# Kernel optimization log

Hardware: AMD Instinct MI355X
Metric: run time of the kernel (lower is better)

Reference implementation:

```python
import jax, jax.numpy as jnp
import numpy as np

T, B, OBS, H, M1, M2, A = 64, 2048, 48, 256, 512, 256, 12
LOG2PI = float(np.log(2.0 * np.pi))
LOG_STD_MIN, LOG_STD_MAX = -5.0, 2.0
LN_EPS = 1e-5


def _elu(x):
    return jnp.where(x > 0, x, jnp.expm1(x))


def setup_inputs() -> dict:
    key = jax.random.key(0)
    ks = jax.random.split(key, 10)
    s = lambda k, shape, sc=0.05: jax.random.normal(k, shape, jnp.float32) * sc
    return dict(
        x=jax.random.normal(ks[0], (T, B, OBS), jnp.float32),
        done=jax.random.randint(ks[1], (T, B), 0, 2).astype(jnp.int32),
        h0=jnp.zeros((B, H), jnp.float32),
        c0=jnp.zeros((B, H), jnp.float32),
        W_ih=s(ks[2], (4 * H, OBS)),
        W_hh=s(ks[3], (4 * H, H)),
        b_ih=jnp.zeros((4 * H,), jnp.float32),
        b_hh=jnp.zeros((4 * H,), jnp.float32),
        ln_g=jnp.ones((H,), jnp.float32),
        ln_b=jnp.zeros((H,), jnp.float32),
        W1=s(ks[4], (H, M1)),
        b1=jnp.zeros((M1,), jnp.float32),
        W2=s(ks[5], (M1, M2)),
        b2=jnp.zeros((M2,), jnp.float32),
        Wm=s(ks[6], (M2, A), 0.01),
        bm=jnp.zeros((A,), jnp.float32),
        Ws=s(ks[7], (M2, A), 0.01),
        bs=jnp.zeros((A,), jnp.float32),
    )


def reference(x, h0, c0, W_ih, W_hh, b_ih, b_hh, ln_g, ln_b,
              W1, b1, W2, b2, Wm, bm, Ws, bs, done):
    # Precompute input-side gate projections for all timesteps: [T, B, 4H]
    xg = jnp.einsum('tbi,gi->tbg', x, W_ih) + b_ih + b_hh
    keep = 1.0 - done.astype(jnp.float32)  # [T, B]; reset state where done==1

    def step(carry, inp):
        h, c = carry
        xgt, m = inp
        h = h * m[:, None]
        c = c * m[:, None]
        g = xgt + h @ W_hh.T  # [B, 4H], PyTorch gate order i,f,g,o
        i, f, gg, o = jnp.split(g, 4, axis=-1)
        c = jax.nn.sigmoid(f) * c + jax.nn.sigmoid(i) * jnp.tanh(gg)
        h = jax.nn.sigmoid(o) * jnp.tanh(c)
        return (h, c), h

    (_, _), hs = jax.lax.scan(step, (h0, c0), (xg, keep))
    hflat = hs.reshape(T * B, H)

    # LayerNorm
    mu = hflat.mean(-1, keepdims=True)
    var = ((hflat - mu) ** 2).mean(-1, keepdims=True)
    y = (hflat - mu) / jnp.sqrt(var + LN_EPS) * ln_g + ln_b

    # Actor MLP (ELU after every Linear, per build_mlp)
    y = _elu(y @ W1 + b1)
    y = _elu(y @ W2 + b2)

    mean = y @ Wm + bm
    logstd = jnp.clip(y @ Ws + bs, LOG_STD_MIN, LOG_STD_MAX)
    # deterministic action == mean, so (a - mu)^2 / (2 sigma^2) == 0
    logp = (-logstd - 0.5 * LOG2PI).sum(-1)
    ent = (0.5 + 0.5 * LOG2PI + logstd).sum(-1)
    # [T*B, A+2]: action mean, log_prob, entropy
    return jnp.concatenate([mean, logp[:, None], ent[:, None]], axis=-1)
```

## Files before the change

kernel.cpp:

```cpp
#include <hip/hip_runtime.h>
#include <hip/hip_bf16.h>
#include <math.h>

#define T_   64
#define B_   2048
#define OBS_ 48
#define H_   256
#define M1_  512
#define M2_  256
#define A_   12
#define BH_  (B_ * H_)
#define KP_  320
#define GROUPS_  128
#define SLICES_  2
#define RPB_     16

typedef unsigned short u16;
typedef unsigned long long u64;
typedef __attribute__((ext_vector_type(8))) short bf16x8;
typedef __attribute__((ext_vector_type(4))) float f32x4;

static __device__ __forceinline__ u16 f2b(float f) {
    __hip_bfloat16 h = __float2bfloat16(f);
    return *reinterpret_cast<u16*>(&h);
}
static __device__ __forceinline__ float b2f(u16 u) {
    union { unsigned u32v; float f; } v; v.u32v = ((unsigned)u) << 16; return v.f;
}
static __device__ __forceinline__ float sigm(float x) {
    return 1.0f / (1.0f + __expf(-x));
}
static __device__ __forceinline__ float tanh_fast(float x) {
    x = fminf(fmaxf(x, -15.0f), 15.0f);
    float e = __expf(2.0f * x);
    return (e - 1.0f) / (e + 1.0f);
}
static __device__ __forceinline__ float elu(float x) {
    return x > 0.0f ? x : (__expf(x) - 1.0f);
}

__global__ void prep_xpad(const float* __restrict__ x, u16* __restrict__ xpad,
                          unsigned* __restrict__ cnt) {
    if (blockIdx.x == 0 && threadIdx.x < GROUPS_ * SLICES_) cnt[threadIdx.x] = 0;
    const int gid = blockIdx.x * 256 + threadIdx.x;
    const int r = gid >> 3, k0 = (gid & 7) * 8;
    u16 tmp[8];
    if (k0 < OBS_) {
        const float4 f0 = *(const float4*)(x + (size_t)r * OBS_ + k0);
        const float4 f1 = *(const float4*)(x + (size_t)r * OBS_ + k0 + 4);
        tmp[0] = f2b(f0.x); tmp[1] = f2b(f0.y); tmp[2] = f2b(f0.z); tmp[3] = f2b(f0.w);
        tmp[4] = f2b(f1.x); tmp[5] = f2b(f1.y); tmp[6] = f2b(f1.z); tmp[7] = f2b(f1.w);
    } else {
        #pragma unroll
        for (int i = 0; i < 8; ++i) tmp[i] = 0;
    }
    *(uint4*)(xpad + (size_t)gid * 8) = *(uint4*)tmp;
}

__global__ void prep_weights(const float* __restrict__ W_ih, const float* __restrict__ W_hh,
                             const float* __restrict__ W1,  const float* __restrict__ W2,
                             const float* __restrict__ Wm,  const float* __restrict__ Ws,
                             u16* __restrict__ Wcat, u16* __restrict__ W1T,
                             u16* __restrict__ W2T,  u16* __restrict__ WhT) {
    const int b = blockIdx.x, tid = threadIdx.x;
    if (b < 1024) {
        const int s = b >> 9, w = (b >> 6) & 7, g = (b >> 4) & 3, jj = b & 15;
        const int src = g * 256 + s * 128 + w * 16 + jj;
        for (int k = tid; k < KP_; k += 256) {
            float v;
            if (k < OBS_)     v = W_ih[src * OBS_ + k];
            else if (k < 64)  v = 0.0f;
            else if (k < 192) v = W_hh[src * H_ + s * 128 + (k - 64)];
            else              v = W_hh[src * H_ + (1 - s) * 128 + (k - 192)];
            Wcat[b * KP_ + k] = f2b(v);
        }
    } else if (b < 1536) {
        const int n = b - 1024;
        W1T[n * 256 + tid] = f2b(W1[tid * M1_ + n]);
    } else if (b < 1792) {
        const int n = b - 1536;
        W2T[n * 512 + tid]       = f2b(W2[tid * M2_ + n]);
        W2T[n * 512 + tid + 256] = f2b(W2[(tid + 256) * M2_ + n]);
    } else {
        const int n = b - 1792;
        float v = 0.0f;
        if (n < 12)                 v = Wm[tid * A_ + n];
        else if (n >= 16 && n < 28) v = Ws[tid * A_ + (n - 16)];
        WhT[n * 256 + tid] = f2b(v);
    }
}

#define ASM_(row, chunk) (a_sm + (size_t)(row) * 320 + (size_t)(((chunk) ^ ((row) & 7)) << 3))

__global__ __launch_bounds__(512, 2) void lstm_sync2(
    const u16*  __restrict__ xpad,
    const int*  __restrict__ done,
    const float* __restrict__ h0,
    const float* __restrict__ c0,
    u16*        __restrict__ hs,
    const u16*  __restrict__ Wcat,
    const float* __restrict__ b_ih,
    const float* __restrict__ b_hh,
    unsigned*   __restrict__ cnt)
{
    __shared__ u16 a_sm[RPB_ * 320];
    __shared__ unsigned okf;

    const int tid  = threadIdx.x;
    const int lane = tid & 63;
    const int w    = tid >> 6;
    const int quad = lane >> 4, l16 = lane & 15;
    const int grp  = blockIdx.x >> 1;
    const int s    = blockIdx.x & 1;
    const int b0   = grp * RPB_;
    const int j    = s * 128 + w * 16 + l16;
    const int jrel = w * 16 + l16;
    const int pc0  = (1 - s) * 128;

    float bsum[4];
    #pragma unroll
    for (int g = 0; g < 4; ++g) bsum[g] = b_ih[g * 256 + j] + b_hh[g * 256 + j];

    float cst[4];
    #pragma unroll
    for (int r = 0; r < 4; ++r) {
        const int row = b0 + quad * 4 + r;
        cst[r] = done[row] ? 0.0f : c0[(size_t)row * H_ + j];
    }

    bf16x8 Bs[4][10];
    #pragma unroll
    for (int g = 0; g < 4; ++g) {
        const u16* wp = Wcat + (size_t)(((s * 8 + w) * 4 + g) * 16 + l16) * KP_ + quad * 8;
        #pragma unroll
        for (int kt = 0; kt < 10; ++kt)
            Bs[g][kt] = *(const bf16x8*)(wp + kt * 32);
    }

    if ((tid & 3) == 0) {
        const int idx = tid >> 2, row = idx >> 3, seg = idx & 7;
        *(uint4*)ASM_(row, seg) =
            *(const uint4*)(xpad + (size_t)(b0 + row) * 64 + seg * 8);
    }
    {
        const int row = tid >> 5, c8 = tid & 31;
        const int cglob = c8 * 8;
        const int dn = done[b0 + row];
        const float* hr = h0 + (size_t)(b0 + row) * H_ + cglob;
        u16 tmp[8];
        #pragma unroll
        for (int e = 0; e < 8; ++e) tmp[e] = dn ? (u16)0 : f2b(hr[e]);
        const int chunk = (((cglob >> 7) == s) ? 8 : 24) + ((cglob & 127) >> 3);
        *(uint4*)ASM_(row, chunk) = *(uint4*)tmp;
    }
    __syncthreads();

    for (int t = 0; t < T_; ++t) {
        unsigned fv = 0;
        if (tid == 0 && t > 0)
            fv = __hip_atomic_load(&cnt[blockIdx.x ^ 1], __ATOMIC_RELAXED,
                                   __HIP_MEMORY_SCOPE_AGENT);

        f32x4 acc[4];
        #pragma unroll
        for (int g = 0; g < 4; ++g) acc[g] = (f32x4){0, 0, 0, 0};
        #pragma unroll
        for (int kt = 0; kt < 6; ++kt) {
            const bf16x8 af = *(const bf16x8*)ASM_(l16, kt * 4 + quad);
            #pragma unroll
            for (int g = 0; g < 4; ++g)
                acc[g] = __builtin_amdgcn_mfma_f32_16x16x32_bf16(af, Bs[g][kt], acc[g], 0, 0, 0);
        }

        if (tid == 0) okf = (t == 0 || fv >= (unsigned)t) ? 1u : 0u;
        __syncthreads();
        {
            int guard = 0;
            while (!okf) {
                if (tid == 0) {
                    __builtin_amdgcn_s_sleep(1);
                    fv = __hip_atomic_load(&cnt[blockIdx.x ^ 1], __ATOMIC_RELAXED,
                                           __HIP_MEMORY_SCOPE_AGENT);
                    if (fv >= (unsigned)t || ++guard > (1 << 22)) okf = 1u;
                }
                __syncthreads();
            }
        }

        if (t > 0 && tid < 256) {
            const u16* hst = hs + (size_t)t * BH_;
            const int row = tid >> 4, q = tid & 15;
            const int dn = done[(size_t)t * B_ + b0 + row];
            uint4 hv = *(const uint4*)(hst + (size_t)(b0 + row) * H_ + pc0 + q * 8);
            if (dn) hv = make_uint4(0u, 0u, 0u, 0u);
            *(uint4*)ASM_(row, 24 + q) = hv;
        }
        if (t + 1 < T_ && tid >= 256 && tid < 384) {
            const int idx = tid - 256, row = idx >> 3, seg = idx & 7;
            *(uint4*)ASM_(row, seg) =
                *(const uint4*)(xpad + ((size_t)(t + 1) * B_ + b0 + row) * 64 + seg * 8);
        }
        __syncthreads();

        #pragma unroll
        for (int kt = 6; kt < 10; ++kt) {
            const bf16x8 af = *(const bf16x8*)ASM_(l16, kt * 4 + quad);
            #pragma unroll
            for (int g = 0; g < 4; ++g)
                acc[g] = __builtin_amdgcn_mfma_f32_16x16x32_bf16(af, Bs[g][kt], acc[g], 0, 0, 0);
        }

        u16* hs1 = hs + (size_t)(t + 1) * BH_;
        #pragma unroll
        for (int r = 0; r < 4; ++r) {
            const int rowl = quad * 4 + r;
            const int rowg = b0 + rowl;
            const float gi = acc[0][r] + bsum[0];
            const float gf = acc[1][r] + bsum[1];
            const float gg = acc[2][r] + bsum[2];
            const float go = acc[3][r] + bsum[3];
            const float cn = sigm(gf) * cst[r] + sigm(gi) * tanh_fast(gg);
            const float h  = sigm(go) * tanh_fast(cn);
            const float kp = (t + 1 < T_)
                ? (done[(size_t)(t + 1) * B_ + rowg] ? 0.0f : 1.0f) : 1.0f;
            cst[r] = cn * kp;
            const int e = 64 + jrel;
            *(ASM_(rowl, e >> 3) + (e & 7)) = f2b(h * kp);
            const unsigned hb = (unsigned)f2b(h);
            const unsigned ob = (unsigned)__shfl_xor((int)hb, 1);
            if ((l16 & 1) == 0) {
                const unsigned val = hb | (ob << 16);
                __hip_atomic_store((unsigned*)(hs1 + (size_t)rowg * H_ + (j & ~1)), val,
                                   __ATOMIC_RELAXED, __HIP_MEMORY_SCOPE_AGENT);
            }
        }
        __syncthreads();

        if (tid == 0 && t + 1 < T_)
            __hip_atomic_store(&cnt[blockIdx.x], (unsigned)(t + 1),
                               __ATOMIC_RELAXED, __HIP_MEMORY_SCOPE_AGENT);
    }
}

#define SY(row, col) ((size_t)(row) * 256 + ((((col) >> 3) ^ ((row) & 7)) << 3) + ((col) & 7))

__global__ __launch_bounds__(512, 4) void mlp_mfma64(
    const u16*  __restrict__ hs,
    float*      __restrict__ out,
    const float* __restrict__ lng, const float* __restrict__ lnb,
    const u16*  __restrict__ W1T, const float* __restrict__ b1,
    const u16*  __restrict__ W2T, const float* __restrict__ b2,
    const u16*  __restrict__ WhT,
    const float* __restrict__ bm, const float* __restrict__ bs)
{
    __shared__ u16 ybf[64 * 256];
    __shared__ u16 yh [64 * 256];

    const int tid  = threadIdx.x;
    const int lane = tid & 63;
    const int wave = tid >> 6;
    const int quad = lane >> 4, l16 = lane & 15;
    const int row0 = blockIdx.x * 64;

    {
        const float4 gv = *(const float4*)(lng + lane * 4);
        const float4 bv = *(const float4*)(lnb + lane * 4);
        #pragma unroll
        for (int rr = 0; rr < 8; ++rr) {
            const int r = wave * 8 + rr;
            const u64 hv8 = __builtin_nontemporal_load(
                (const u64*)(hs + (size_t)(row0 + r) * H_ + lane * 4));
            const u16 h0v = (u16)(hv8 & 0xffff), h1v = (u16)((hv8 >> 16) & 0xffff);
            const u16 h2v = (u16)((hv8 >> 32) & 0xffff), h3v = (u16)(hv8 >> 48);
            const float v0 = b2f(h0v), v1 = b2f(h1v), v2 = b2f(h2v), v3 = b2f(h3v);
            float s  = v0 + v1 + v2 + v3;
            float ss = v0 * v0 + v1 * v1 + v2 * v2 + v3 * v3;
            #pragma unroll
            for (int off = 32; off > 0; off >>= 1) {
                s  += __shfl_down(s,  off);
                ss += __shfl_down(ss, off);
            }
            s = __shfl(s, 0); ss = __shfl(ss, 0);
            const float mu   = s * (1.0f / 256.0f);
            const float rstd = rsqrtf(ss * (1.0f / 256.0f) - mu * mu + 1e-5f);
            ushort4 o;
            o.x = f2b((v0 - mu) * rstd * gv.x + bv.x);
            o.y = f2b((v1 - mu) * rstd * gv.y + bv.y);
            o.z = f2b((v2 - mu) * rstd * gv.z + bv.z);
            o.w = f2b((v3 - mu) * rstd * gv.w + bv.w);
            *(ushort4*)(ybf + SY(r, lane * 4)) = o;
        }
    }
    __syncthreads();

    f32x4 acc2[4][2];
    #pragma unroll
    for (int m = 0; m < 4; ++m)
        #pragma unroll
        for (int j = 0; j < 2; ++j) acc2[m][j] = (f32x4){0,0,0,0};

    #pragma unroll
    for (int ph = 0; ph < 2; ++ph) {
        {
            f32x4 acc[4][2];
            #pragma unroll
            for (int m = 0; m < 4; ++m)
                #pragma unroll
                for (int j = 0; j < 2; ++j) acc[m][j] = (f32x4){0,0,0,0};
            const int n0 = ph * 256 + wave * 32;
            const u16* wp0 = W1T + (size_t)(n0 + l16) * 256 + quad * 8;
            const u16* wp1 = W1T + (size_t)(n0 + 16 + l16) * 256 + quad * 8;
            #pragma unroll
            for (int kt = 0; kt < 8; ++kt) {
                const int k0 = kt * 32;
                const bf16x8 bw0 = *(const bf16x8*)(wp0 + k0);
                const bf16x8 bw1 = *(const bf16x8*)(wp1 + k0);
                #pragma unroll
                for (int m = 0; m < 4; ++m) {
                    const bf16x8 af = *(const bf16x8*)(ybf + SY(m * 16 + l16, k0 + quad * 8));
                    acc[m][0] = __builtin_amdgcn_mfma_f32_16x16x32_bf16(af, bw0, acc[m][0], 0, 0, 0);
                    acc[m][1] = __builtin_amdgcn_mfma_f32_16x16x32_bf16(af, bw1, acc[m][1], 0, 0, 0);
                }
            }
            const float bb0 = b1[n0 + l16], bb1 = b1[n0 + 16 + l16];
            __syncthreads();
            #pragma unroll
            for (int m = 0; m < 4; ++m)
                #pragma unroll
                for (int r = 0; r < 4; ++r) {
                    const int row = m * 16 + quad * 4 + r;
                    yh[SY(row, wave * 32 + l16)]      = f2b(elu(acc[m][0][r] + bb0));
                    yh[SY(row, wave * 32 + 16 + l16)] = f2b(elu(acc[m][1][r] + bb1));
                }
        }
        __syncthreads();

        {
            const int n0 = wave * 32;
            const u16* wp0 = W2T + (size_t)(n0 + l16) * 512 + ph * 256 + quad * 8;
            const u16* wp1 = W2T + (size_t)(n0 + 16 + l16) * 512 + ph * 256 + quad * 8;
            #pragma unroll
            for (int kt = 0; kt < 8; ++kt) {
                const int k0 = kt * 32;
                const bf16x8 bw0 = *(const bf16x8*)(wp0 + k0);
                const bf16x8 bw1 = *(const bf16x8*)(wp1 + k0);
                #pragma unroll
                for (int m = 0; m < 4; ++m) {
                    const bf16x8 af = *(const bf16x8*)(yh + SY(m * 16 + l16, k0 + quad * 8));
                    acc2[m][0] = __builtin_amdgcn_mfma_f32_16x16x32_bf16(af, bw0, acc2[m][0], 0, 0, 0);
                    acc2[m][1] = __builtin_amdgcn_mfma_f32_16x16x32_bf16(af, bw1, acc2[m][1], 0, 0, 0);
                }
            }
        }
        __syncthreads();
    }

    {
        const float bb0 = b2[wave * 32 + l16], bb1 = b2[wave * 32 + 16 + l16];
        #pragma unroll
        for (int m = 0; m < 4; ++m)
            #pragma unroll
            for (int r = 0; r < 4; ++r) {
                const int row = m * 16 + quad * 4 + r;
                ybf[SY(row, wave * 32 + l16)]      = f2b(elu(acc2[m][0][r] + bb0));
                ybf[SY(row, wave * 32 + 16 + l16)] = f2b(elu(acc2[m][1][r] + bb1));
            }
    }
    __syncthreads();

    float* lsf = (float*)yh;
    if (wave < 4) {
        f32x4 a0 = {0,0,0,0}, a1 = {0,0,0,0};
        const u16* wp0 = WhT + (size_t)l16 * 256 + quad * 8;
        const u16* wp1 = WhT + (size_t)(16 + l16) * 256 + quad * 8;
        #pragma unroll
        for (int kt = 0; kt < 8; ++kt) {
            const int k0 = kt * 32;
            const bf16x8 af  = *(const bf16x8*)(ybf + SY(wave * 16 + l16, k0 + quad * 8));
            const bf16x8 bw0 = *(const bf16x8*)(wp0 + k0);
            const bf16x8 bw1 = *(const bf16x8*)(wp1 + k0);
            a0 = __builtin_amdgcn_mfma_f32_16x16x32_bf16(af, bw0, a0, 0, 0, 0);
            a1 = __builtin_amdgcn_mfma_f32_16x16x32_bf16(af, bw1, a1, 0, 0, 0);
        }
        if (l16 < 12) {
            const float bbm = bm[l16], bbs = bs[l16];
            #pragma unroll
            for (int r = 0; r < 4; ++r) {
                const int row = wave * 16 + quad * 4 + r;
                out[(size_t)(row0 + row) * 14 + l16] = a0[r] + bbm;
                lsf[row * 16 + l16] = fminf(fmaxf(a1[r] + bbs, -5.0f), 2.0f);
            }
        }
    }
    __syncthreads();
    if (tid < 64) {
        float s = 0.0f;
        #pragma unroll
        for (int q = 0; q < 12; ++q) s += lsf[tid * 16 + q];
        const float LOG2PI = 1.8378770664093453f;
        out[(size_t)(row0 + tid) * 14 + 12] = -s - 6.0f * LOG2PI;
        out[(size_t)(row0 + tid) * 14 + 13] =  s + 6.0f + 6.0f * LOG2PI;
    }
}

extern "C" void kernel_launch(void* const* d_in, const int* in_sizes, int n_in,
                              void* d_out, int out_size, void* d_ws, size_t ws_size,
                              hipStream_t stream) {
    (void)in_sizes; (void)n_in; (void)out_size; (void)ws_size;
    const float* x    = (const float*)d_in[0];
    const int*   done = (const int*)  d_in[1];
    const float* h0   = (const float*)d_in[2];
    const float* c0   = (const float*)d_in[3];
    const float* W_ih = (const float*)d_in[4];
    const float* W_hh = (const float*)d_in[5];
    const float* b_ih = (const float*)d_in[6];
    const float* b_hh = (const float*)d_in[7];
    const float* lng  = (const float*)d_in[8];
    const float* lnb  = (const float*)d_in[9];
    const float* W1   = (const float*)d_in[10];
    const float* b1   = (const float*)d_in[11];
    const float* W2   = (const float*)d_in[12];
    const float* b2   = (const float*)d_in[13];
    const float* Wm   = (const float*)d_in[14];
    const float* bm   = (const float*)d_in[15];
    const float* Ws   = (const float*)d_in[16];
    const float* bs   = (const float*)d_in[17];
    float* out = (float*)d_out;

    unsigned char* p = (unsigned char*)d_ws;
    u16* hs    = (u16*)p;              p += (size_t)(T_ + 1) * BH_ * 2;
    u16* xpad  = (u16*)p;              p += (size_t)T_ * B_ * 64 * 2;
    u16* Wcat  = (u16*)p;              p += (size_t)1024 * KP_ * 2;
    u16* W1T   = (u16*)p;              p += (size_t)M1_ * H_ * 2;
    u16* W2T   = (u16*)p;              p += (size_t)M2_ * M1_ * 2;
    u16* WhT   = (u16*)p;              p += (size_t)32 * H_ * 2;
    unsigned* cnt = (unsigned*)p;      p += 1024;

    prep_xpad<<<(T_ * B_ * 8) / 256, 256, 0, stream>>>(x, xpad, cnt);
    prep_weights<<<1824, 256, 0, stream>>>(W_ih, W_hh, W1, W2, Wm, Ws,
                                           Wcat, W1T, W2T, WhT);

    lstm_sync2<<<GROUPS_ * SLICES_, 512, 0, stream>>>(
        xpad, done, h0, c0, hs, Wcat, b_ih, b_hh, cnt);

    mlp_mfma64<<<(T_ * B_) / 64, 512, 0, stream>>>(
        hs + BH_, out, lng, lnb, W1T, b1, W2T, b2, WhT, bm, bs);
}
```

Before: 581.4 us.

## Restructure LSTM step sync: wait at step end, double-buffer x, prefetch h

The LSTM kernel now waits on the partner block's counter at the end of each step instead of mid-step. This removes the mid-step spin loop and one of the two block barriers per step. The x input is double-buffered in shared memory, and the partner's h slice and the next x tile are loaded into registers before the first MFMA batch, hiding global latency behind compute. The blocks are also remapped so partner slices are 128 blocks apart, and the two prep kernels are fused into one launch. The trade-offs are more shared memory per block and a reliance on the end-of-step wait to make the partner's hs writes visible to the early loads.

Result: slower. 598.1 us (+2.9%).

```diff
diff --git a/kernel.cpp b/kernel.cpp
--- a/kernel.cpp
+++ b/kernel.cpp
@@ -39,30 +39,32 @@
     return x > 0.0f ? x : (__expf(x) - 1.0f);
 }
 
-__global__ void prep_xpad(const float* __restrict__ x, u16* __restrict__ xpad,
-                          unsigned* __restrict__ cnt) {
-    if (blockIdx.x == 0 && threadIdx.x < GROUPS_ * SLICES_) cnt[threadIdx.x] = 0;
-    const int gid = blockIdx.x * 256 + threadIdx.x;
-    const int r = gid >> 3, k0 = (gid & 7) * 8;
-    u16 tmp[8];
-    if (k0 < OBS_) {
-        const float4 f0 = *(const float4*)(x + (size_t)r * OBS_ + k0);
-        const float4 f1 = *(const float4*)(x + (size_t)r * OBS_ + k0 + 4);
-        tmp[0] = f2b(f0.x); tmp[1] = f2b(f0.y); tmp[2] = f2b(f0.z); tmp[3] = f2b(f0.w);
-        tmp[4] = f2b(f1.x); tmp[5] = f2b(f1.y); tmp[6] = f2b(f1.z); tmp[7] = f2b(f1.w);
-    } else {
-        #pragma unroll
-        for (int i = 0; i < 8; ++i) tmp[i] = 0;
-    }
-    *(uint4*)(xpad + (size_t)gid * 8) = *(uint4*)tmp;
-}
-
-__global__ void prep_weights(const float* __restrict__ W_ih, const float* __restrict__ W_hh,
-                             const float* __restrict__ W1,  const float* __restrict__ W2,
-                             const float* __restrict__ Wm,  const float* __restrict__ Ws,
-                             u16* __restrict__ Wcat, u16* __restrict__ W1T,
-                             u16* __restrict__ W2T,  u16* __restrict__ WhT) {
-    const int b = blockIdx.x, tid = threadIdx.x;
+__global__ void prep_all(const float* __restrict__ x, u16* __restrict__ xpad,
+                         const float* __restrict__ W_ih, const float* __restrict__ W_hh,
+                         const float* __restrict__ W1,  const float* __restrict__ W2,
+                         const float* __restrict__ Wm,  const float* __restrict__ Ws,
+                         u16* __restrict__ Wcat, u16* __restrict__ W1T,
+                         u16* __restrict__ W2T,  u16* __restrict__ WhT,
+                         unsigned* __restrict__ cnt) {
+    const int blk = blockIdx.x, tid = threadIdx.x;
+    if (blk < 4096) {
+        const int gid = blk * 256 + tid;
+        const int r = gid >> 3, k0 = (gid & 7) * 8;
+        u16 tmp[8];
+        if (k0 < OBS_) {
+            const float4 f0 = *(const float4*)(x + (size_t)r * OBS_ + k0);
+            const float4 f1 = *(const float4*)(x + (size_t)r * OBS_ + k0 + 4);
+            tmp[0] = f2b(f0.x); tmp[1] = f2b(f0.y); tmp[2] = f2b(f0.z); tmp[3] = f2b(f0.w);
+            tmp[4] = f2b(f1.x); tmp[5] = f2b(f1.y); tmp[6] = f2b(f1.z); tmp[7] = f2b(f1.w);
+        } else {
+            #pragma unroll
+            for (int i = 0; i < 8; ++i) tmp[i] = 0;
+        }
+        *(uint4*)(xpad + (size_t)gid * 8) = *(uint4*)tmp;
+        return;
+    }
+    const int b = blk - 4096;
+    if (b == 0 && tid < GROUPS_ * SLICES_) cnt[tid] = 0;
     if (b < 1024) {
         const int s = b >> 9, w = (b >> 6) & 7, g = (b >> 4) & 3, jj = b & 15;
         const int src = g * 256 + s * 128 + w * 16 + jj;
@@ -90,9 +92,9 @@
     }
 }
 
-#define ASM_(row, chunk) (a_sm + (size_t)(row) * 320 + (size_t)(((chunk) ^ ((row) & 7)) << 3))
-
-__global__ __launch_bounds__(512, 2) void lstm_sync2(
+#define ASM_(row, chunk) (a_sm + (size_t)(row) * 384 + (size_t)(((chunk) ^ ((row) & 7)) << 3))
+
+__global__ __launch_bounds__(512, 2) void lstm_sync3(
     const u16*  __restrict__ xpad,
     const int*  __restrict__ done,
     const float* __restrict__ h0,
@@ -103,15 +105,15 @@
     const float* __restrict__ b_hh,
     unsigned*   __restrict__ cnt)
 {
-    __shared__ u16 a_sm[RPB_ * 320];
-    __shared__ unsigned okf;
+    __shared__ u16 a_sm[RPB_ * 384];
 
     const int tid  = threadIdx.x;
     const int lane = tid & 63;
     const int w    = tid >> 6;
     const int quad = lane >> 4, l16 = lane & 15;
-    const int grp  = blockIdx.x >> 1;
-    const int s    = blockIdx.x & 1;
+    const int grp  = blockIdx.x & 127;
+    const int s    = blockIdx.x >> 7;
+    const int pidx = blockIdx.x ^ 128;
     const int b0   = grp * RPB_;
     const int j    = s * 128 + w * 16 + l16;
     const int jrel = w * 16 + l16;
@@ -150,61 +152,58 @@
         u16 tmp[8];
         #pragma unroll
         for (int e = 0; e < 8; ++e) tmp[e] = dn ? (u16)0 : f2b(hr[e]);
-        const int chunk = (((cglob >> 7) == s) ? 8 : 24) + ((cglob & 127) >> 3);
+        const int chunk = (((cglob >> 7) == s) ? 16 : 32) + ((cglob & 127) >> 3);
         *(uint4*)ASM_(row, chunk) = *(uint4*)tmp;
     }
     __syncthreads();
 
     for (int t = 0; t < T_; ++t) {
-        unsigned fv = 0;
-        if (tid == 0 && t > 0)
-            fv = __hip_atomic_load(&cnt[blockIdx.x ^ 1], __ATOMIC_RELAXED,
-                                   __HIP_MEMORY_SCOPE_AGENT);
+        const int xb  = (t & 1) * 8;
+        const int xbn = ((t + 1) & 1) * 8;
+
+        uint4 hstage; int hrow = 0, hq = 0;
+        const bool do_h = (t > 0) && (tid < 256);
+        if (do_h) {
+            hrow = tid >> 4; hq = tid & 15;
+            hstage = *(const uint4*)(hs + (size_t)t * BH_ +
+                                     (size_t)(b0 + hrow) * H_ + pc0 + hq * 8);
+        }
+        uint4 xstage; int xrow = 0, xseg = 0;
+        const bool do_x = (t + 1 < T_) && (tid >= 256 && tid < 384);
+        if (do_x) {
+            const int idx = tid - 256; xrow = idx >> 3; xseg = idx & 7;
+            xstage = *(const uint4*)(xpad + ((size_t)(t + 1) * B_ + b0 + xrow) * 64 + xseg * 8);
+        }
 
         f32x4 acc[4];
         #pragma unroll
         for (int g = 0; g < 4; ++g) acc[g] = (f32x4){0, 0, 0, 0};
         #pragma unroll
-        for (int kt = 0; kt < 6; ++kt) {
-            const bf16x8 af = *(const bf16x8*)ASM_(l16, kt * 4 + quad);
+        for (int kt = 0; kt < 2; ++kt) {
+            const bf16x8 af = *(const bf16x8*)ASM_(l16, xb + kt * 4 + quad);
             #pragma unroll
             for (int g = 0; g < 4; ++g)
                 acc[g] = __builtin_amdgcn_mfma_f32_16x16x32_bf16(af, Bs[g][kt], acc[g], 0, 0, 0);
         }
-
-        if (tid == 0) okf = (t == 0 || fv >= (unsigned)t) ? 1u : 0u;
+        #pragma unroll
+        for (int kt = 2; kt < 6; ++kt) {
+            const bf16x8 af = *(const bf16x8*)ASM_(l16, 16 + (kt - 2) * 4 + quad);
+            #pragma unroll
+            for (int g = 0; g < 4; ++g)
+                acc[g] = __builtin_amdgcn_mfma_f32_16x16x32_bf16(af, Bs[g][kt], acc[g], 0, 0, 0);
+        }
+
+        if (do_h) {
+            const int dn = done[(size_t)t * B_ + b0 + hrow];
+            if (dn) hstage = make_uint4(0u, 0u, 0u, 0u);
+            *(uint4*)ASM_(hrow, 32 + hq) = hstage;
+        }
+        if (do_x) *(uint4*)ASM_(xrow, xbn + xseg) = xstage;
         __syncthreads();
-        {
-            int guard = 0;
-            while (!okf) {
-                if (tid == 0) {
-                    __builtin_amdgcn_s_sleep(1);
-                    fv = __hip_atomic_load(&cnt[blockIdx.x ^ 1], __ATOMIC_RELAXED,
-                                           __HIP_MEMORY_SCOPE_AGENT);
-                    if (fv >= (unsigned)t || ++guard > (1 << 22)) okf = 1u;
-                }
-                __syncthreads();
-            }
-        }
-
-        if (t > 0 && tid < 256) {
-            const u16* hst = hs + (size_t)t * BH_;
-            const int row = tid >> 4, q = tid & 15;
-            const int dn = done[(size_t)t * B_ + b0 + row];
-            uint4 hv = *(const uint4*)(hst + (size_t)(b0 + row) * H_ + pc0 + q * 8);
-            if (dn) hv = make_uint4(0u, 0u, 0u, 0u);
-            *(uint4*)ASM_(row, 24 + q) = hv;
-        }
-        if (t + 1 < T_ && tid >= 256 && tid < 384) {
-            const int idx = tid - 256, row = idx >> 3, seg = idx & 7;
-            *(uint4*)ASM_(row, seg) =
-                *(const uint4*)(xpad + ((size_t)(t + 1) * B_ + b0 + row) * 64 + seg * 8);
-        }
-        __syncthreads();
 
         #pragma unroll
         for (int kt = 6; kt < 10; ++kt) {
-            const bf16x8 af = *(const bf16x8*)ASM_(l16, kt * 4 + quad);
+            const bf16x8 af = *(const bf16x8*)ASM_(l16, 32 + (kt - 6) * 4 + quad);
             #pragma unroll
             for (int g = 0; g < 4; ++g)
                 acc[g] = __builtin_amdgcn_mfma_f32_16x16x32_bf16(af, Bs[g][kt], acc[g], 0, 0, 0);
@@ -224,8 +223,7 @@
             const float kp = (t + 1 < T_)
                 ? (done[(size_t)(t + 1) * B_ + rowg] ? 0.0f : 1.0f) : 1.0f;
             cst[r] = cn * kp;
-            const int e = 64 + jrel;
-            *(ASM_(rowl, e >> 3) + (e & 7)) = f2b(h * kp);
+            *(ASM_(rowl, 16 + (jrel >> 3)) + (jrel & 7)) = f2b(h * kp);
             const unsigned hb = (unsigned)f2b(h);
             const unsigned ob = (unsigned)__shfl_xor((int)hb, 1);
             if ((l16 & 1) == 0) {
@@ -236,9 +234,19 @@
         }
         __syncthreads();
 
-        if (tid == 0 && t + 1 < T_)
-            __hip_atomic_store(&cnt[blockIdx.x], (unsigned)(t + 1),
-                               __ATOMIC_RELAXED, __HIP_MEMORY_SCOPE_AGENT);
+        if (t + 1 < T_) {
+            if (tid == 0) {
+                __hip_atomic_store(&cnt[blockIdx.x], (unsigned)(t + 1),
+                                   __ATOMIC_RELAXED, __HIP_MEMORY_SCOPE_AGENT);
+                int guard = 0;
+                while (__hip_atomic_load(&cnt[pidx], __ATOMIC_RELAXED,
+                                         __HIP_MEMORY_SCOPE_AGENT) < (unsigned)(t + 1)) {
+                    __builtin_amdgcn_s_sleep(1);
+                    if (++guard > (1 << 22)) break;
+                }
+            }
+            __syncthreads();
+        }
     }
 }
 
@@ -436,11 +444,10 @@
     u16* WhT   = (u16*)p;              p += (size_t)32 * H_ * 2;
     unsigned* cnt = (unsigned*)p;      p += 1024;
 
-    prep_xpad<<<(T_ * B_ * 8) / 256, 256, 0, stream>>>(x, xpad, cnt);
-    prep_weights<<<1824, 256, 0, stream>>>(W_ih, W_hh, W1, W2, Wm, Ws,
-                                           Wcat, W1T, W2T, WhT);
-
-    lstm_sync2<<<GROUPS_ * SLICES_, 512, 0, stream>>>(
+    prep_all<<<4096 + 1824, 256, 0, stream>>>(x, xpad, W_ih, W_hh, W1, W2, Wm, Ws,
+                                              Wcat, W1T, W2T, WhT, cnt);
+
+    lstm_sync3<<<GROUPS_ * SLICES_, 512, 0, stream>>>(
         xpad, done, h0, c0, hs, Wcat, b_ih, b_hh, cnt);
 
     mlp_mfma64<<<(T_ * B_) / 64, 512, 0, stream>>>(
```

## Fuse LSTM scan and MLP into one persistent kernel with per-timestep flags

Applied to the files above, without the earlier changes.

Merges the two prep kernels into one launch. Also merges the LSTM scan and the MLP head into one launch: the first 256 blocks run the recurrent scan, and the remaining blocks each spin on the per-group progress counters until the timestep they need is done, then run LayerNorm and the MLP. This lets MLP work overlap the serial scan instead of waiting for it to finish, and removes launch gaps. In exchange, every block uses 64KB of shared memory, which may lower occupancy for the scan blocks. It also relies on the scan blocks being scheduled ahead of the spinning MLP blocks to avoid deadlock, with a guard counter as a fallback.

After: 577.0 us. Within noise of the previous version (-0.7%).

```diff
diff --git a/kernel.cpp b/kernel.cpp
--- a/kernel.cpp
+++ b/kernel.cpp
@@ -14,6 +14,8 @@
 #define GROUPS_  128
 #define SLICES_  2
 #define RPB_     16
+#define NSCAN_   (GROUPS_ * SLICES_)
+#define NMLP_    ((T_ * B_) / 64)
 
 typedef unsigned short u16;
 typedef unsigned long long u64;
@@ -39,30 +41,32 @@
     return x > 0.0f ? x : (__expf(x) - 1.0f);
 }
 
-__global__ void prep_xpad(const float* __restrict__ x, u16* __restrict__ xpad,
-                          unsigned* __restrict__ cnt) {
-    if (blockIdx.x == 0 && threadIdx.x < GROUPS_ * SLICES_) cnt[threadIdx.x] = 0;
-    const int gid = blockIdx.x * 256 + threadIdx.x;
-    const int r = gid >> 3, k0 = (gid & 7) * 8;
-    u16 tmp[8];
-    if (k0 < OBS_) {
-        const float4 f0 = *(const float4*)(x + (size_t)r * OBS_ + k0);
-        const float4 f1 = *(const float4*)(x + (size_t)r * OBS_ + k0 + 4);
-        tmp[0] = f2b(f0.x); tmp[1] = f2b(f0.y); tmp[2] = f2b(f0.z); tmp[3] = f2b(f0.w);
-        tmp[4] = f2b(f1.x); tmp[5] = f2b(f1.y); tmp[6] = f2b(f1.z); tmp[7] = f2b(f1.w);
-    } else {
-        #pragma unroll
-        for (int i = 0; i < 8; ++i) tmp[i] = 0;
-    }
-    *(uint4*)(xpad + (size_t)gid * 8) = *(uint4*)tmp;
-}
-
-__global__ void prep_weights(const float* __restrict__ W_ih, const float* __restrict__ W_hh,
-                             const float* __restrict__ W1,  const float* __restrict__ W2,
-                             const float* __restrict__ Wm,  const float* __restrict__ Ws,
-                             u16* __restrict__ Wcat, u16* __restrict__ W1T,
-                             u16* __restrict__ W2T,  u16* __restrict__ WhT) {
-    const int b = blockIdx.x, tid = threadIdx.x;
+__global__ void prep_all(const float* __restrict__ x, u16* __restrict__ xpad,
+                         const float* __restrict__ W_ih, const float* __restrict__ W_hh,
+                         const float* __restrict__ W1,  const float* __restrict__ W2,
+                         const float* __restrict__ Wm,  const float* __restrict__ Ws,
+                         u16* __restrict__ Wcat, u16* __restrict__ W1T,
+                         u16* __restrict__ W2T,  u16* __restrict__ WhT,
+                         unsigned* __restrict__ cnt) {
+    const int blk = blockIdx.x, tid = threadIdx.x;
+    if (blk < 4096) {
+        const int gid = blk * 256 + tid;
+        const int r = gid >> 3, k0 = (gid & 7) * 8;
+        u16 tmp[8];
+        if (k0 < OBS_) {
+            const float4 f0 = *(const float4*)(x + (size_t)r * OBS_ + k0);
+            const float4 f1 = *(const float4*)(x + (size_t)r * OBS_ + k0 + 4);
+            tmp[0] = f2b(f0.x); tmp[1] = f2b(f0.y); tmp[2] = f2b(f0.z); tmp[3] = f2b(f0.w);
+            tmp[4] = f2b(f1.x); tmp[5] = f2b(f1.y); tmp[6] = f2b(f1.z); tmp[7] = f2b(f1.w);
+        } else {
+            #pragma unroll
+            for (int i = 0; i < 8; ++i) tmp[i] = 0;
+        }
+        *(uint4*)(xpad + (size_t)gid * 8) = *(uint4*)tmp;
+        return;
+    }
+    const int b = blk - 4096;
+    if (b == 0 && tid < NSCAN_) cnt[tid] = 0;
     if (b < 1024) {
         const int s = b >> 9, w = (b >> 6) & 7, g = (b >> 4) & 3, jj = b & 15;
         const int src = g * 256 + s * 128 + w * 16 + jj;
@@ -91,8 +95,9 @@
 }
 
 #define ASM_(row, chunk) (a_sm + (size_t)(row) * 320 + (size_t)(((chunk) ^ ((row) & 7)) << 3))
-
-__global__ __launch_bounds__(512, 2) void lstm_sync2(
+#define SY(row, col) ((size_t)(row) * 256 + ((((col) >> 3) ^ ((row) & 7)) << 3) + ((col) & 7))
+
+__global__ __launch_bounds__(512, 2) void scan_mlp(
     const u16*  __restrict__ xpad,
     const int*  __restrict__ done,
     const float* __restrict__ h0,
@@ -101,151 +106,7 @@
     const u16*  __restrict__ Wcat,
     const float* __restrict__ b_ih,
     const float* __restrict__ b_hh,
-    unsigned*   __restrict__ cnt)
-{
-    __shared__ u16 a_sm[RPB_ * 320];
-    __shared__ unsigned okf;
-
-    const int tid  = threadIdx.x;
-    const int lane = tid & 63;
-    const int w    = tid >> 6;
-    const int quad = lane >> 4, l16 = lane & 15;
-    const int grp  = blockIdx.x >> 1;
-    const int s    = blockIdx.x & 1;
-    const int b0   = grp * RPB_;
-    const int j    = s * 128 + w * 16 + l16;
-    const int jrel = w * 16 + l16;
-    const int pc0  = (1 - s) * 128;
-
-    float bsum[4];
-    #pragma unroll
-    for (int g = 0; g < 4; ++g) bsum[g] = b_ih[g * 256 + j] + b_hh[g * 256 + j];
-
-    float cst[4];
-    #pragma unroll
-    for (int r = 0; r < 4; ++r) {
-        const int row = b0 + quad * 4 + r;
-        cst[r] = done[row] ? 0.0f : c0[(size_t)row * H_ + j];
-    }
-
-    bf16x8 Bs[4][10];
-    #pragma unroll
-    for (int g = 0; g < 4; ++g) {
-        const u16* wp = Wcat + (size_t)(((s * 8 + w) * 4 + g) * 16 + l16) * KP_ + quad * 8;
-        #pragma unroll
-        for (int kt = 0; kt < 10; ++kt)
-            Bs[g][kt] = *(const bf16x8*)(wp + kt * 32);
-    }
-
-    if ((tid & 3) == 0) {
-        const int idx = tid >> 2, row = idx >> 3, seg = idx & 7;
-        *(uint4*)ASM_(row, seg) =
-            *(const uint4*)(xpad + (size_t)(b0 + row) * 64 + seg * 8);
-    }
-    {
-        const int row = tid >> 5, c8 = tid & 31;
-        const int cglob = c8 * 8;
-        const int dn = done[b0 + row];
-        const float* hr = h0 + (size_t)(b0 + row) * H_ + cglob;
-        u16 tmp[8];
-        #pragma unroll
-        for (int e = 0; e < 8; ++e) tmp[e] = dn ? (u16)0 : f2b(hr[e]);
-        const int chunk = (((cglob >> 7) == s) ? 8 : 24) + ((cglob & 127) >> 3);
-        *(uint4*)ASM_(row, chunk) = *(uint4*)tmp;
-    }
-    __syncthreads();
-
-    for (int t = 0; t < T_; ++t) {
-        unsigned fv = 0;
-        if (tid == 0 && t > 0)
-            fv = __hip_atomic_load(&cnt[blockIdx.x ^ 1], __ATOMIC_RELAXED,
-                                   __HIP_MEMORY_SCOPE_AGENT);
-
-        f32x4 acc[4];
-        #pragma unroll
-        for (int g = 0; g < 4; ++g) acc[g] = (f32x4){0, 0, 0, 0};
-        #pragma unroll
-        for (int kt = 0; kt < 6; ++kt) {
-            const bf16x8 af = *(const bf16x8*)ASM_(l16, kt * 4 + quad);
-            #pragma unroll
-            for (int g = 0; g < 4; ++g)
-                acc[g] = __builtin_amdgcn_mfma_f32_16x16x32_bf16(af, Bs[g][kt], acc[g], 0, 0, 0);
-        }
-
-        if (tid == 0) okf = (t == 0 || fv >= (unsigned)t) ? 1u : 0u;
-        __syncthreads();
-        {
-            int guard = 0;
-            while (!okf) {
-                if (tid == 0) {
-                    __builtin_amdgcn_s_sleep(1);
-                    fv = __hip_atomic_load(&cnt[blockIdx.x ^ 1], __ATOMIC_RELAXED,
-                                           __HIP_MEMORY_SCOPE_AGENT);
-                    if (fv >= (unsigned)t || ++guard > (1 << 22)) okf = 1u;
-                }
-                __syncthreads();
-            }
-        }
-
-        if (t > 0 && tid < 256) {
-            const u16* hst = hs + (size_t)t * BH_;
-            const int row = tid >> 4, q = tid & 15;
-            const int dn = done[(size_t)t * B_ + b0 + row];
-            uint4 hv = *(const uint4*)(hst + (size_t)(b0 + row) * H_ + pc0 + q * 8);
-            if (dn) hv = make_uint4(0u, 0u, 0u, 0u);
-            *(uint4*)ASM_(row, 24 + q) = hv;
-        }
-        if (t + 1 < T_ && tid >= 256 && tid < 384) {
-            const int idx = tid - 256, row = idx >> 3, seg = idx & 7;
-            *(uint4*)ASM_(row, seg) =
-                *(const uint4*)(xpad + ((size_t)(t + 1) * B_ + b0 + row) * 64 + seg * 8);
-        }
-        __syncthreads();
-
-        #pragma unroll
-        for (int kt = 6; kt < 10; ++kt) {
-            const bf16x8 af = *(const bf16x8*)ASM_(l16, kt * 4 + quad);
-            #pragma unroll
-            for (int g = 0; g < 4; ++g)
-                acc[g] = __builtin_amdgcn_mfma_f32_16x16x32_bf16(af, Bs[g][kt], acc[g], 0, 0, 0);
-        }
-
-        u16* hs1 = hs + (size_t)(t + 1) * BH_;
-        #pragma unroll
-        for (int r = 0; r < 4; ++r) {
-            const int rowl = quad * 4 + r;
-            const int rowg = b0 + rowl;
-            const float gi = acc[0][r] + bsum[0];
-            const float gf = acc[1][r] + bsum[1];
-            const float gg = acc[2][r] + bsum[2];
-            const float go = acc[3][r] + bsum[3];
-            const float cn = sigm(gf) * cst[r] + sigm(gi) * tanh_fast(gg);
-            const float h  = sigm(go) * tanh_fast(cn);
-            const float kp = (t + 1 < T_)
-                ? (done[(size_t)(t + 1) * B_ + rowg] ? 0.0f : 1.0f) : 1.0f;
-            cst[r] = cn * kp;
-            const int e = 64 + jrel;
-            *(ASM_(rowl, e >> 3) + (e & 7)) = f2b(h * kp);
-            const unsigned hb = (unsigned)f2b(h);
-            const unsigned ob = (unsigned)__shfl_xor((int)hb, 1);
-            if ((l16 & 1) == 0) {
-                const unsigned val = hb | (ob << 16);
-                __hip_atomic_store((unsigned*)(hs1 + (size_t)rowg * H_ + (j & ~1)), val,
-                                   __ATOMIC_RELAXED, __HIP_MEMORY_SCOPE_AGENT);
-            }
-        }
-        __syncthreads();
-
-        if (tid == 0 && t + 1 < T_)
-            __hip_atomic_store(&cnt[blockIdx.x], (unsigned)(t + 1),
-                               __ATOMIC_RELAXED, __HIP_MEMORY_SCOPE_AGENT);
-    }
-}
-
-#define SY(row, col) ((size_t)(row) * 256 + ((((col) >> 3) ^ ((row) & 7)) << 3) + ((col) & 7))
-
-__global__ __launch_bounds__(512, 4) void mlp_mfma64(
-    const u16*  __restrict__ hs,
+    unsigned*   __restrict__ cnt,
     float*      __restrict__ out,
     const float* __restrict__ lng, const float* __restrict__ lnb,
     const u16*  __restrict__ W1T, const float* __restrict__ b1,
@@ -253,14 +114,171 @@
     const u16*  __restrict__ WhT,
     const float* __restrict__ bm, const float* __restrict__ bs)
 {
-    __shared__ u16 ybf[64 * 256];
-    __shared__ u16 yh [64 * 256];
+    __shared__ u16 smem[32768];
+    __shared__ unsigned okf;
 
     const int tid  = threadIdx.x;
     const int lane = tid & 63;
+    const int quad = (lane >> 4), l16 = lane & 15;
+
+    if (blockIdx.x < NSCAN_) {
+        u16* a_sm = smem;
+        const int w    = tid >> 6;
+        const int grp  = blockIdx.x >> 1;
+        const int s    = blockIdx.x & 1;
+        const int pidx = blockIdx.x ^ 1;
+        const int b0   = grp * RPB_;
+        const int j    = s * 128 + w * 16 + l16;
+        const int jrel = w * 16 + l16;
+        const int pc0  = (1 - s) * 128;
+
+        float bsum[4];
+        #pragma unroll
+        for (int g = 0; g < 4; ++g) bsum[g] = b_ih[g * 256 + j] + b_hh[g * 256 + j];
+
+        float cst[4];
+        #pragma unroll
+        for (int r = 0; r < 4; ++r) {
+            const int row = b0 + quad * 4 + r;
+            cst[r] = done[row] ? 0.0f : c0[(size_t)row * H_ + j];
+        }
+
+        bf16x8 Bs[4][10];
+        #pragma unroll
+        for (int g = 0; g < 4; ++g) {
+            const u16* wp = Wcat + (size_t)(((s * 8 + w) * 4 + g) * 16 + l16) * KP_ + quad * 8;
+            #pragma unroll
+            for (int kt = 0; kt < 10; ++kt)
+                Bs[g][kt] = *(const bf16x8*)(wp + kt * 32);
+        }
+
+        if ((tid & 3) == 0) {
+            const int idx = tid >> 2, row = idx >> 3, seg = idx & 7;
+            *(uint4*)ASM_(row, seg) =
+                *(const uint4*)(xpad + (size_t)(b0 + row) * 64 + seg * 8);
+        }
+        {
+            const int row = tid >> 5, c8 = tid & 31;
+            const int cglob = c8 * 8;
+            const int dn = done[b0 + row];
+            const float* hr = h0 + (size_t)(b0 + row) * H_ + cglob;
+            u16 tmp[8];
+            #pragma unroll
+            for (int e = 0; e < 8; ++e) tmp[e] = dn ? (u16)0 : f2b(hr[e]);
+            const int chunk = (((cglob >> 7) == s) ? 8 : 24) + ((cglob & 127) >> 3);
+            *(uint4*)ASM_(row, chunk) = *(uint4*)tmp;
+        }
+        __syncthreads();
+
+        for (int t = 0; t < T_; ++t) {
+            unsigned fv = 0;
+            if (tid == 0 && t > 0)
+                fv = __hip_atomic_load(&cnt[pidx], __ATOMIC_RELAXED,
+                                       __HIP_MEMORY_SCOPE_AGENT);
+
+            f32x4 acc[4];
+            #pragma unroll
+            for (int g = 0; g < 4; ++g) acc[g] = (f32x4){0, 0, 0, 0};
+            #pragma unroll
+            for (int kt = 0; kt < 6; ++kt) {
+                const bf16x8 af = *(const bf16x8*)ASM_(l16, kt * 4 + quad);
+                #pragma unroll
+                for (int g = 0; g < 4; ++g)
+                    acc[g] = __builtin_amdgcn_mfma_f32_16x16x32_bf16(af, Bs[g][kt], acc[g], 0, 0, 0);
+            }
+
+            if (tid == 0) okf = (t == 0 || fv >= (unsigned)t) ? 1u : 0u;
+            __syncthreads();
+            {
+                int guard = 0;
+                while (!okf) {
+                    if (tid == 0) {
+                        __builtin_amdgcn_s_sleep(1);
+                        fv = __hip_atomic_load(&cnt[pidx], __ATOMIC_RELAXED,
+                                               __HIP_MEMORY_SCOPE_AGENT);
+                        if (fv >= (unsigned)t || ++guard > (1 << 22)) okf = 1u;
+                    }
+                    __syncthreads();
+                }
+            }
+
+            if (t > 0 && tid < 256) {
+                const u16* hst = hs + (size_t)t * BH_;
+                const int row = tid >> 4, q = tid & 15;
+                const int dn = done[(size_t)t * B_ + b0 + row];
+                uint4 hv = *(const uint4*)(hst + (size_t)(b0 + row) * H_ + pc0 + q * 8);
+                if (dn) hv = make_uint4(0u, 0u, 0u, 0u);
+                *(uint4*)ASM_(row, 24 + q) = hv;
+            }
+            if (t + 1 < T_ && tid >= 256 && tid < 384) {
+                const int idx = tid - 256, row = idx >> 3, seg = idx & 7;
+                *(uint4*)ASM_(row, seg) =
+                    *(const uint4*)(xpad + ((size_t)(t + 1) * B_ + b0 + row) * 64 + seg * 8);
+            }
+            __syncthreads();
+
+            #pragma unroll
+            for (int kt = 6; kt < 10; ++kt) {
+                const bf16x8 af = *(const bf16x8*)ASM_(l16, kt * 4 + quad);
+                #pragma unroll
+                for (int g = 0; g < 4; ++g)
+                    acc[g] = __builtin_amdgcn_mfma_f32_16x16x32_bf16(af, Bs[g][kt], acc[g], 0, 0, 0);
+            }
+
+            u16* hs1 = hs + (size_t)(t + 1) * BH_;
+            #pragma unroll
+            for (int r = 0; r < 4; ++r) {
+                const int rowl = quad * 4 + r;
+                const int rowg = b0 + rowl;
+                const float gi = acc[0][r] + bsum[0];
+                const float gf = acc[1][r] + bsum[1];
+                const float gg = acc[2][r] + bsum[2];
+                const float go = acc[3][r] + bsum[3];
+                const float cn = sigm(gf) * cst[r] + sigm(gi) * tanh_fast(gg);
+                const float h  = sigm(go) * tanh_fast(cn);
+                const float kp = (t + 1 < T_)
+                    ? (done[(size_t)(t + 1) * B_ + rowg] ? 0.0f : 1.0f) : 1.0f;
+                cst[r] = cn * kp;
+                const int e = 64 + jrel;
+                *(ASM_(rowl, e >> 3) + (e & 7)) = f2b(h * kp);
+                const unsigned hb = (unsigned)f2b(h);
+                const unsigned ob = (unsigned)__shfl_xor((int)hb, 1);
+                if ((l16 & 1) == 0) {
+                    const unsigned val = hb | (ob << 16);
+                    __hip_atomic_store((unsigned*)(hs1 + (size_t)rowg * H_ + (j & ~1)), val,
+                                       __ATOMIC_RELAXED, __HIP_MEMORY_SCOPE_AGENT);
+                }
+            }
+            __syncthreads();
+
+            if (tid == 0)
+                __hip_atomic_store(&cnt[blockIdx.x], (unsigned)(t + 1),
+                                   __ATOMIC_RELAXED, __HIP_MEMORY_SCOPE_AGENT);
+        }
+        return;
+    }
+
+    u16* ybf = smem;
+    u16* yh  = smem + 16384;
     const int wave = tid >> 6;
-    const int quad = lane >> 4, l16 = lane & 15;
-    const int row0 = blockIdx.x * 64;
+    const int mbid = blockIdx.x - NSCAN_;
+    const int row0 = mbid * 64;
+    const u16* hsr = hs + BH_;
+
+    {
+        const int ts = row0 / B_ + 1;
+        const int g0 = (row0 % B_) / RPB_;
+        if (tid < 8) {
+            const int grp = g0 + (tid >> 1), s = tid & 1;
+            int guard = 0;
+            while (__hip_atomic_load(&cnt[grp * 2 + s], __ATOMIC_RELAXED,
+                                     __HIP_MEMORY_SCOPE_AGENT) < (unsigned)ts) {
+                __builtin_amdgcn_s_sleep(2);
+                if (++guard > (1 << 20)) break;
+            }
+        }
+        __syncthreads();
+    }
 
     {
         const float4 gv = *(const float4*)(lng + lane * 4);
@@ -269,7 +287,7 @@
         for (int rr = 0; rr < 8; ++rr) {
             const int r = wave * 8 + rr;
             const u64 hv8 = __builtin_nontemporal_load(
-                (const u64*)(hs + (size_t)(row0 + r) * H_ + lane * 4));
+                (const u64*)(hsr + (size_t)(row0 + r) * H_ + lane * 4));
             const u16 h0v = (u16)(hv8 & 0xffff), h1v = (u16)((hv8 >> 16) & 0xffff);
             const u16 h2v = (u16)((hv8 >> 32) & 0xffff), h3v = (u16)(hv8 >> 48);
             const float v0 = b2f(h0v), v1 = b2f(h1v), v2 = b2f(h2v), v3 = b2f(h3v);
@@ -297,7 +315,7 @@
     #pragma unroll
     for (int m = 0; m < 4; ++m)
         #pragma unroll
-        for (int j = 0; j < 2; ++j) acc2[m][j] = (f32x4){0,0,0,0};
+        for (int jj = 0; jj < 2; ++jj) acc2[m][jj] = (f32x4){0,0,0,0};
 
     #pragma unroll
     for (int ph = 0; ph < 2; ++ph) {
@@ -306,7 +324,7 @@
             #pragma unroll
             for (int m = 0; m < 4; ++m)
                 #pragma unroll
-                for (int j = 0; j < 2; ++j) acc[m][j] = (f32x4){0,0,0,0};
+                for (int jj = 0; jj < 2; ++jj) acc[m][jj] = (f32x4){0,0,0,0};
             const int n0 = ph * 256 + wave * 32;
             const u16* wp0 = W1T + (size_t)(n0 + l16) * 256 + quad * 8;
             const u16* wp1 = W1T + (size_t)(n0 + 16 + l16) * 256 + quad * 8;
@@ -436,13 +454,10 @@
     u16* WhT   = (u16*)p;              p += (size_t)32 * H_ * 2;
     unsigned* cnt = (unsigned*)p;      p += 1024;
 
-    prep_xpad<<<(T_ * B_ * 8) / 256, 256, 0, stream>>>(x, xpad, cnt);
-    prep_weights<<<1824, 256, 0, stream>>>(W_ih, W_hh, W1, W2, Wm, Ws,
-                                           Wcat, W1T, W2T, WhT);
-
-    lstm_sync2<<<GROUPS_ * SLICES_, 512, 0, stream>>>(
-        xpad, done, h0, c0, hs, Wcat, b_ih, b_hh, cnt);
-
-    mlp_mfma64<<<(T_ * B_) / 64, 512, 0, stream>>>(
-        hs + BH_, out, lng, lnb, W1T, b1, W2T, b2, WhT, bm, bs);
-}
+    prep_all<<<4096 + 1824, 256, 0, stream>>>(x, xpad, W_ih, W_hh, W1, W2, Wm, Ws,
+                                              Wcat, W1T, W2T, WhT, cnt);
+
+    scan_mlp<<<NSCAN_ + NMLP_, 512, 0, stream>>>(
+        xpad, done, h0, c0, hs, Wcat, b_ih, b_hh, cnt,
+        out, lng, lnb, W1T, b1, W2T, b2, WhT, bm, bs);
+}
```
